# Performance work log

Measured on AMD Instinct MI355X. Metric: run time of the kernel, lower is better.

## Reference

```python
import jax, jax.numpy as jnp
import numpy as np

N = 50000
E_RAND = 800000
F_IN = 256
F_OUT = 256
ALPHA = 0.2  # LeakyReLU negative slope


def setup_inputs() -> dict:
    key = jax.random.key(0)
    k1, k2, k3, k4 = jax.random.split(key, 4)
    x = jax.random.normal(k1, (N, F_IN), dtype=jnp.float32)
    # random edges + self-loops so every row has at least one edge (avoids div by 0)
    edge_rand = jax.random.randint(k2, (2, E_RAND), 0, N)
    loops = jnp.arange(N)
    edge = jnp.concatenate([edge_rand, jnp.stack([loops, loops])], axis=1)  # [2, 850000]
    W = jax.random.normal(k3, (F_IN, F_OUT), dtype=jnp.float32) * 0.05
    a = jax.random.normal(k4, (2 * F_OUT,), dtype=jnp.float32) * 0.05
    return {"x": x, "edge": edge, "W": W, "a": a}


def reference(x, edge, W, a):
    # x: [N, F_in], edge: [2, E] (row = dst/aggregation index per torch.sparse.mm(a, h))
    n = x.shape[0]
    f_out = W.shape[1]
    h = x @ W  # [N, F_out]
    src, dst = edge[0], edge[1]
    # a @ [h_src; h_dst] decomposes into two per-node dot products (no [E, 2F] concat)
    s = h @ a[:f_out]   # [N]
    t = h @ a[f_out:]   # [N]
    logit = s[src] + t[dst]                                  # [E]
    e = jnp.exp(-jax.nn.leaky_relu(logit, ALPHA))            # [E]
    rowsum = jax.ops.segment_sum(e, src, num_segments=n)     # [N]
    msg = e[:, None] * h[dst]                                # [E, F_out]
    h_prime = jax.ops.segment_sum(msg, src, num_segments=n)  # [N, F_out]
    h_prime = h_prime / rowsum[:, None]
    return jax.nn.relu(h_prime)  # concat=True path
```

## Files before the change

### kernel.cpp

```cpp
#include <hip/hip_runtime.h>
#include <hip/hip_fp16.h>

#define FDIM 256
#define ALPHA 0.2f

typedef _Float16 half8 __attribute__((ext_vector_type(8)));
typedef float floatx4 __attribute__((ext_vector_type(4)));

__global__ __launch_bounds__(256) void prep_hist(const float* __restrict__ W,
                                                 _Float16* __restrict__ wswz,
                                                 const int* __restrict__ edge,
                                                 int* __restrict__ deg, int E) {
  if (blockIdx.x < 32) {
    const int g = blockIdx.x * 256 + threadIdx.x;
    const int kc = g >> 11, L = g & 2047;
    const int n = L >> 3, c = L & 7;
    half8 hv;
#pragma unroll
    for (int j = 0; j < 8; ++j)
      hv[j] = (_Float16)W[(size_t)(kc * 64 + c * 8 + j) * 256 + n];
    *(half8*)(wswz + (size_t)g * 8) = hv;
  } else {
    const int e = (blockIdx.x - 32) * 256 + threadIdx.x;
    if (e < E) atomicAdd(&deg[edge[e]], 1);
  }
}

#define HT_STRIDE 264
__global__ __launch_bounds__(256) void gemm_mfma(
    const float* __restrict__ x, const _Float16* __restrict__ wswz,
    const float* __restrict__ a, _Float16* __restrict__ h,
    float* __restrict__ s, float* __restrict__ t, int M) {
  __shared__ __align__(16) _Float16 smem[64 * HT_STRIDE];
  _Float16* As = smem;
  const int tid = threadIdx.x;
  const int w = tid >> 6, l = tid & 63;
  const int l15 = l & 15, q = l >> 4;
  const int row0 = blockIdx.x * 64;

  floatx4 acc[4][4];
#pragma unroll
  for (int mt = 0; mt < 4; ++mt)
#pragma unroll
    for (int nt = 0; nt < 4; ++nt) acc[mt][nt] = (floatx4){0.f, 0.f, 0.f, 0.f};

  const int id0 = tid, id1 = 256 + tid;
  const int m0 = id0 >> 3, c0 = (id0 & 7) ^ (m0 & 7);
  const int m1 = id1 >> 3, c1 = (id1 & 7) ^ (m1 & 7);
  const int r0 = row0 + m0, r1 = row0 + m1;

  float4 pf[2][2];
  auto loadA = [&](int kc) {
    pf[0][0] = pf[0][1] = pf[1][0] = pf[1][1] = make_float4(0.f, 0.f, 0.f, 0.f);
    if (r0 < M) {
      const float4* p = (const float4*)(x + (size_t)r0 * 256 + kc * 64 + c0 * 8);
      pf[0][0] = p[0];
      pf[0][1] = p[1];
    }
    if (r1 < M) {
      const float4* p = (const float4*)(x + (size_t)r1 * 256 + kc * 64 + c1 * 8);
      pf[1][0] = p[0];
      pf[1][1] = p[1];
    }
  };
  auto storeA = [&]() {
#pragma unroll
    for (int hf = 0; hf < 2; ++hf) {
      half8 hv;
      hv[0] = (_Float16)pf[hf][0].x; hv[1] = (_Float16)pf[hf][0].y;
      hv[2] = (_Float16)pf[hf][0].z; hv[3] = (_Float16)pf[hf][0].w;
      hv[4] = (_Float16)pf[hf][1].x; hv[5] = (_Float16)pf[hf][1].y;
      hv[6] = (_Float16)pf[hf][1].z; hv[7] = (_Float16)pf[hf][1].w;
      *(half8*)(As + (size_t)(hf * 256 + tid) * 8) = hv;
    }
  };

  loadA(0);
  for (int kc = 0; kc < 4; ++kc) {
    storeA();
    half8 bf[2][4];
#pragma unroll
    for (int ks = 0; ks < 2; ++ks) {
      const int c = ks * 4 + q;
#pragma unroll
      for (int nt = 0; nt < 4; ++nt) {
        const int n = w * 64 + nt * 16 + l15;
        bf[ks][nt] = *(const half8*)(wswz + (size_t)(kc * 2048 + n * 8 + c) * 8);
      }
    }
    __syncthreads();
    if (kc < 3) loadA(kc + 1);
#pragma unroll
    for (int ks = 0; ks < 2; ++ks) {
      const int c = ks * 4 + q;
      half8 af[4];
#pragma unroll
      for (int mt = 0; mt < 4; ++mt) {
        const int m = mt * 16 + l15;
        af[mt] = *(const half8*)(As + (size_t)(m * 8 + (c ^ (m & 7))) * 8);
      }
#pragma unroll
      for (int mt = 0; mt < 4; ++mt)
#pragma unroll
        for (int nt = 0; nt < 4; ++nt)
          acc[mt][nt] = __builtin_amdgcn_mfma_f32_16x16x32_f16(
              af[mt], bf[ks][nt], acc[mt][nt], 0, 0, 0);
    }
    __syncthreads();
  }

#pragma unroll
  for (int mt = 0; mt < 4; ++mt)
#pragma unroll
    for (int nt = 0; nt < 4; ++nt)
#pragma unroll
      for (int r = 0; r < 4; ++r)
        smem[(size_t)(mt * 16 + q * 4 + r) * HT_STRIDE + w * 64 + nt * 16 +
             l15] = (_Float16)acc[mt][nt][r];
  __syncthreads();

  const int w8 = tid >> 5;
  const int colh = (tid & 31) * 8;
#pragma unroll
  for (int p = 0; p < 8; ++p) {
    const int rl = p * 8 + w8;
    const int row = row0 + rl;
    if (row < M)
      *(half8*)(h + (size_t)row * 256 + colh) =
          *(const half8*)(smem + (size_t)rl * HT_STRIDE + colh);
  }

  const int r8 = tid >> 2, seg = tid & 3;
  float sp = 0.f, tp = 0.f;
#pragma unroll
  for (int c8 = 0; c8 < 8; ++c8) {
    const int col = seg * 64 + c8 * 8;
    const half8 hv = *(const half8*)(smem + (size_t)r8 * HT_STRIDE + col);
    const float4 a0 = *(const float4*)(a + col);
    const float4 a1 = *(const float4*)(a + col + 4);
    const float4 b0 = *(const float4*)(a + 256 + col);
    const float4 b1 = *(const float4*)(a + 256 + col + 4);
    sp += (float)hv[0] * a0.x + (float)hv[1] * a0.y + (float)hv[2] * a0.z +
          (float)hv[3] * a0.w + (float)hv[4] * a1.x + (float)hv[5] * a1.y +
          (float)hv[6] * a1.z + (float)hv[7] * a1.w;
    tp += (float)hv[0] * b0.x + (float)hv[1] * b0.y + (float)hv[2] * b0.z +
          (float)hv[3] * b0.w + (float)hv[4] * b1.x + (float)hv[5] * b1.y +
          (float)hv[6] * b1.z + (float)hv[7] * b1.w;
  }
  sp += __shfl_xor(sp, 1);
  sp += __shfl_xor(sp, 2);
  tp += __shfl_xor(tp, 1);
  tp += __shfl_xor(tp, 2);
  if (seg == 0 && row0 + r8 < M) {
    s[row0 + r8] = sp;
    t[row0 + r8] = tp;
  }
}

__global__ __launch_bounds__(1024) void scan1(const int* __restrict__ deg,
                                              int* __restrict__ rowstart,
                                              int* __restrict__ bsum, int n) {
  const int tid = threadIdx.x;
  const int i = blockIdx.x * 1024 + tid;
  const int val = (i < n) ? deg[i] : 0;
  const int lane = tid & 63, wv = tid >> 6;
  int v = val;
#pragma unroll
  for (int off = 1; off < 64; off <<= 1) {
    const int o = __shfl_up(v, off);
    if (lane >= off) v += o;
  }
  __shared__ int wsum[16];
  __shared__ int woff[16];
  if (lane == 63) wsum[wv] = v;
  __syncthreads();
  if (tid < 16) {
    int wv2 = wsum[tid];
#pragma unroll
    for (int off = 1; off < 16; off <<= 1) {
      const int o = __shfl_up(wv2, off);
      if (tid >= off) wv2 += o;
    }
    woff[tid] = wv2;
  }
  __syncthreads();
  const int incl = v + (wv ? woff[wv - 1] : 0);
  if (i < n) rowstart[i] = incl - val;
  if (tid == 1023) bsum[blockIdx.x] = woff[15];
}

__global__ __launch_bounds__(64) void scan2(const int* __restrict__ bsum,
                                            int* __restrict__ boff,
                                            int* __restrict__ rowstart, int nb,
                                            int n) {
  const int tid = threadIdx.x;
  int v = (tid < nb) ? bsum[tid] : 0;
#pragma unroll
  for (int off = 1; off < 64; off <<= 1) {
    const int o = __shfl_up(v, off);
    if (tid >= off) v += o;
  }
  if (tid < nb) boff[tid] = v;
  if (tid == nb - 1) rowstart[n] = v;
}

__global__ __launch_bounds__(1024) void scan3(int* __restrict__ rowstart,
                                              int* __restrict__ rsc,
                                              const int* __restrict__ boff,
                                              int n) {
  const int i = blockIdx.x * 1024 + threadIdx.x;
  if (i < n) {
    const int v = rowstart[i] + (blockIdx.x ? boff[blockIdx.x - 1] : 0);
    rowstart[i] = v;
    rsc[i] = v;
  }
}

__global__ void scatter_kernel(const int* __restrict__ edge,
                               int* __restrict__ rsc, int* __restrict__ sdst,
                               int E) {
  const int e = blockIdx.x * 256 + threadIdx.x;
  if (e < E) {
    const int src = edge[e];
    const int dst = edge[E + e];
    const int pos = atomicAdd(&rsc[src], 1);
    sdst[pos] = dst;
  }
}

__global__ __launch_bounds__(256) void agg_kernel(
    const _Float16* __restrict__ h, const float* __restrict__ s,
    const float* __restrict__ t, const int* __restrict__ rowstart,
    const int* __restrict__ sdst, float* __restrict__ out, int n) {
  const int w = threadIdx.x >> 6, l = threadIdx.x & 63;
  const int row = blockIdx.x * 4 + w;
  if (row >= n) return;
  const int start = rowstart[row], end = rowstart[row + 1];
  const float srow = s[row];
  const int half = l >> 5;
  const int lh = l & 31;
  const size_t fo = (size_t)lh * 8;
  float acc[8] = {};
  float rs = 0.f;
  int j = start;
  for (; j + 8 <= end; j += 8) {
#pragma unroll
    for (int u = 0; u < 4; ++u) {
      const int d = sdst[j + u * 2 + half];
      const float logit = srow + t[d];
      const float lr = logit > 0.f ? logit : ALPHA * logit;
      const float e = __expf(-lr);
      const half8 v = *(const half8*)(h + (size_t)d * 256 + fo);
      rs += e;
#pragma unroll
      for (int k = 0; k < 8; ++k) acc[k] += e * (float)v[k];
    }
  }
  for (; j < end; j += 2) {
    const int idx = j + half;
    const bool valid = idx < end;
    const int d = valid ? sdst[idx] : 0;
    const float logit = srow + t[d];
    const float lr = logit > 0.f ? logit : ALPHA * logit;
    const float e = valid ? __expf(-lr) : 0.f;
    const half8 v = *(const half8*)(h + (size_t)d * 256 + fo);
    rs += e;
#pragma unroll
    for (int k = 0; k < 8; ++k) acc[k] += e * (float)v[k];
  }
  rs += __shfl_xor(rs, 32);
#pragma unroll
  for (int k = 0; k < 8; ++k) acc[k] += __shfl_xor(acc[k], 32);
  const float inv = 1.f / rs;
  float4 o;
#pragma unroll
  for (int k = 0; k < 4; ++k) {
    const float vv = acc[half * 4 + k] * inv;
    (&o.x)[k] = vv > 0.f ? vv : 0.f;
  }
  *(float4*)(out + (size_t)row * 256 + lh * 8 + half * 4) = o;
}

extern "C" void kernel_launch(void* const* d_in, const int* in_sizes, int n_in,
                              void* d_out, int out_size, void* d_ws,
                              size_t ws_size, hipStream_t stream) {
  const float* x = (const float*)d_in[0];
  const int* edge = (const int*)d_in[1];
  const float* W = (const float*)d_in[2];
  const float* a = (const float*)d_in[3];
  float* out = (float*)d_out;
  const int N = in_sizes[0] / FDIM;
  const int E = in_sizes[1] / 2;
  const int NB = (N + 1023) / 1024;

  _Float16* h = (_Float16*)d_ws;
  _Float16* wswz = h + (size_t)N * FDIM;
  float* s = (float*)(wswz + 8192 * 8);
  float* t = s + N;
  int* deg = (int*)(t + N);
  int* rsc = deg + N;
  int* rowstart = rsc + N;
  int* bsum = rowstart + N + 2;
  int* boff = bsum + 64;
  int* sdst = boff + 64;

  hipMemsetAsync(deg, 0, (size_t)N * sizeof(int), stream);

  prep_hist<<<32 + (E + 255) / 256, 256, 0, stream>>>(W, wswz, edge, deg, E);
  gemm_mfma<<<(N + 63) / 64, 256, 0, stream>>>(x, wswz, a, h, s, t, N);
  scan1<<<NB, 1024, 0, stream>>>(deg, rowstart, bsum, N);
  scan2<<<1, 64, 0, stream>>>(bsum, boff, rowstart, NB, N);
  scan3<<<NB, 1024, 0, stream>>>(rowstart, rsc, boff, N);
  scatter_kernel<<<(E + 255) / 256, 256, 0, stream>>>(edge, rsc, sdst, E);
  agg_kernel<<<(N + 3) / 4, 256, 0, stream>>>(h, s, t, rowstart, sdst, out, N);
}
```

Baseline: 286.0 us.

## Load full A tile upfront in GEMM and fold scan2 into scan3

The GEMM kernel now loads and converts all four K-chunks of the 64-row x tile into shared memory at once, then runs the MFMA loop with a single barrier instead of a per-chunk double-buffered register prefetch with two barriers per chunk. This removes intra-loop synchronisation and lets all global loads issue together. The cost is that the GEMM can no longer overlap the next chunk's loads with compute. Separately, the single-block scan2 launch is removed: each scan3 block reduces the block sums itself with wave shuffles, saving one kernel launch.

```diff
diff --git a/kernel.cpp b/kernel.cpp
--- a/kernel.cpp
+++ b/kernel.cpp
@@ -44,70 +44,56 @@
 #pragma unroll
     for (int nt = 0; nt < 4; ++nt) acc[mt][nt] = (floatx4){0.f, 0.f, 0.f, 0.f};
 
-  const int id0 = tid, id1 = 256 + tid;
-  const int m0 = id0 >> 3, c0 = (id0 & 7) ^ (m0 & 7);
-  const int m1 = id1 >> 3, c1 = (id1 & 7) ^ (m1 & 7);
-  const int r0 = row0 + m0, r1 = row0 + m1;
-
-  float4 pf[2][2];
-  auto loadA = [&](int kc) {
-    pf[0][0] = pf[0][1] = pf[1][0] = pf[1][1] = make_float4(0.f, 0.f, 0.f, 0.f);
-    if (r0 < M) {
-      const float4* p = (const float4*)(x + (size_t)r0 * 256 + kc * 64 + c0 * 8);
-      pf[0][0] = p[0];
-      pf[0][1] = p[1];
-    }
-    if (r1 < M) {
-      const float4* p = (const float4*)(x + (size_t)r1 * 256 + kc * 64 + c1 * 8);
-      pf[1][0] = p[0];
-      pf[1][1] = p[1];
-    }
-  };
-  auto storeA = [&]() {
+#pragma unroll
+  for (int kc = 0; kc < 4; ++kc)
 #pragma unroll
     for (int hf = 0; hf < 2; ++hf) {
+      const int id = hf * 256 + tid;
+      const int m = id >> 3;
+      const int c = (id & 7) ^ (m & 7);
+      const int row = row0 + m;
+      float4 f0 = make_float4(0.f, 0.f, 0.f, 0.f);
+      float4 f1 = make_float4(0.f, 0.f, 0.f, 0.f);
+      if (row < M) {
+        const float4* p =
+            (const float4*)(x + (size_t)row * 256 + kc * 64 + c * 8);
+        f0 = p[0];
+        f1 = p[1];
+      }
       half8 hv;
-      hv[0] = (_Float16)pf[hf][0].x; hv[1] = (_Float16)pf[hf][0].y;
-      hv[2] = (_Float16)pf[hf][0].z; hv[3] = (_Float16)pf[hf][0].w;
-      hv[4] = (_Float16)pf[hf][1].x; hv[5] = (_Float16)pf[hf][1].y;
-      hv[6] = (_Float16)pf[hf][1].z; hv[7] = (_Float16)pf[hf][1].w;
-      *(half8*)(As + (size_t)(hf * 256 + tid) * 8) = hv;
-    }
-  };
-
-  loadA(0);
-  for (int kc = 0; kc < 4; ++kc) {
-    storeA();
-    half8 bf[2][4];
-#pragma unroll
-    for (int ks = 0; ks < 2; ++ks) {
-      const int c = ks * 4 + q;
-#pragma unroll
-      for (int nt = 0; nt < 4; ++nt) {
-        const int n = w * 64 + nt * 16 + l15;
-        bf[ks][nt] = *(const half8*)(wswz + (size_t)(kc * 2048 + n * 8 + c) * 8);
-      }
-    }
-    __syncthreads();
-    if (kc < 3) loadA(kc + 1);
-#pragma unroll
-    for (int ks = 0; ks < 2; ++ks) {
-      const int c = ks * 4 + q;
-      half8 af[4];
-#pragma unroll
-      for (int mt = 0; mt < 4; ++mt) {
-        const int m = mt * 16 + l15;
-        af[mt] = *(const half8*)(As + (size_t)(m * 8 + (c ^ (m & 7))) * 8);
-      }
-#pragma unroll
-      for (int mt = 0; mt < 4; ++mt)
-#pragma unroll
-        for (int nt = 0; nt < 4; ++nt)
-          acc[mt][nt] = __builtin_amdgcn_mfma_f32_16x16x32_f16(
-              af[mt], bf[ks][nt], acc[mt][nt], 0, 0, 0);
-    }
-    __syncthreads();
-  }
+      hv[0] = (_Float16)f0.x; hv[1] = (_Float16)f0.y;
+      hv[2] = (_Float16)f0.z; hv[3] = (_Float16)f0.w;
+      hv[4] = (_Float16)f1.x; hv[5] = (_Float16)f1.y;
+      hv[6] = (_Float16)f1.z; hv[7] = (_Float16)f1.w;
+      *(half8*)(As + (size_t)(kc * 512 + id) * 8) = hv;
+    }
+  __syncthreads();
+
+#pragma unroll 2
+  for (int ks = 0; ks < 8; ++ks) {
+    const int kc = ks >> 1;
+    const int c = (ks & 1) * 4 + q;
+    half8 bf[4];
+#pragma unroll
+    for (int nt = 0; nt < 4; ++nt) {
+      const int n = w * 64 + nt * 16 + l15;
+      bf[nt] = *(const half8*)(wswz + (size_t)(kc * 2048 + n * 8 + c) * 8);
+    }
+    half8 af[4];
+#pragma unroll
+    for (int mt = 0; mt < 4; ++mt) {
+      const int m = mt * 16 + l15;
+      af[mt] =
+          *(const half8*)(As + (size_t)(kc * 512 + m * 8 + (c ^ (m & 7))) * 8);
+    }
+#pragma unroll
+    for (int mt = 0; mt < 4; ++mt)
+#pragma unroll
+      for (int nt = 0; nt < 4; ++nt)
+        acc[mt][nt] = __builtin_amdgcn_mfma_f32_16x16x32_f16(
+            af[mt], bf[nt], acc[mt][nt], 0, 0, 0);
+  }
+  __syncthreads();
 
 #pragma unroll
   for (int mt = 0; mt < 4; ++mt)
@@ -189,28 +175,30 @@
   if (tid == 1023) bsum[blockIdx.x] = woff[15];
 }
 
-__global__ __launch_bounds__(64) void scan2(const int* __restrict__ bsum,
-                                            int* __restrict__ boff,
-                                            int* __restrict__ rowstart, int nb,
-                                            int n) {
-  const int tid = threadIdx.x;
-  int v = (tid < nb) ? bsum[tid] : 0;
-#pragma unroll
-  for (int off = 1; off < 64; off <<= 1) {
-    const int o = __shfl_up(v, off);
-    if (tid >= off) v += o;
-  }
-  if (tid < nb) boff[tid] = v;
-  if (tid == nb - 1) rowstart[n] = v;
-}
-
 __global__ __launch_bounds__(1024) void scan3(int* __restrict__ rowstart,
                                               int* __restrict__ rsc,
-                                              const int* __restrict__ boff,
-                                              int n) {
-  const int i = blockIdx.x * 1024 + threadIdx.x;
+                                              const int* __restrict__ bsum,
+                                              int n, int nb) {
+  __shared__ int sboff;
+  const int tid = threadIdx.x;
+  if (tid < 64) {
+    const int v = (tid < nb) ? bsum[tid] : 0;
+    int pre = (tid < (int)blockIdx.x) ? v : 0;
+    int tot = v;
+#pragma unroll
+    for (int off = 32; off > 0; off >>= 1) {
+      pre += __shfl_xor(pre, off);
+      tot += __shfl_xor(tot, off);
+    }
+    if (tid == 0) {
+      sboff = pre;
+      if (blockIdx.x == (unsigned)(nb - 1)) rowstart[n] = tot;
+    }
+  }
+  __syncthreads();
+  const int i = blockIdx.x * 1024 + tid;
   if (i < n) {
-    const int v = rowstart[i] + (blockIdx.x ? boff[blockIdx.x - 1] : 0);
+    const int v = rowstart[i] + sboff;
     rowstart[i] = v;
     rsc[i] = v;
   }
@@ -301,16 +289,14 @@
   int* rsc = deg + N;
   int* rowstart = rsc + N;
   int* bsum = rowstart + N + 2;
-  int* boff = bsum + 64;
-  int* sdst = boff + 64;
+  int* sdst = bsum + 64;
 
   hipMemsetAsync(deg, 0, (size_t)N * sizeof(int), stream);
 
   prep_hist<<<32 + (E + 255) / 256, 256, 0, stream>>>(W, wswz, edge, deg, E);
   gemm_mfma<<<(N + 63) / 64, 256, 0, stream>>>(x, wswz, a, h, s, t, N);
   scan1<<<NB, 1024, 0, stream>>>(deg, rowstart, bsum, N);
-  scan2<<<1, 64, 0, stream>>>(bsum, boff, rowstart, NB, N);
-  scan3<<<NB, 1024, 0, stream>>>(rowstart, rsc, boff, N);
+  scan3<<<NB, 1024, 0, stream>>>(rowstart, rsc, bsum, N, NB);
   scatter_kernel<<<(E + 255) / 256, 256, 0, stream>>>(edge, rsc, sdst, E);
   agg_kernel<<<(N + 3) / 4, 256, 0, stream>>>(h, s, t, rowstart, sdst, out, N);
 }
```

Result: no change. 287.8 us (+0.6%).
